# Optimization experiments

Measured on AMD Instinct MI355X. Metric: run time of the kernel, lower is better.

## Reference

```python
import jax, jax.numpy as jnp
import numpy as np

NUM_HEADS = 12


def setup_inputs() -> dict:
    key = jax.random.key(0)
    k1, k2, k3 = jax.random.split(key, 3)
    B, N, C = 2, 2048, 768
    x = jax.random.normal(k1, (B, N, C), dtype=jnp.float32)
    w_qkv = jax.random.normal(k2, (C, 3 * C), dtype=jnp.float32) * 0.02
    w_proj = jax.random.normal(k3, (C, C), dtype=jnp.float32) * 0.02
    b_proj = jnp.zeros((C,), dtype=jnp.float32)
    return {"x": x, "w_qkv": w_qkv, "w_proj": w_proj, "b_proj": b_proj}


def reference(x, w_qkv, w_proj, b_proj):
    B, N, C = x.shape
    H = NUM_HEADS
    D = C // H
    qkv = (x @ w_qkv).reshape(B, N, 3, H, D)  # [B,N,3,H,D]
    q = jnp.transpose(qkv[:, :, 0], (0, 2, 1, 3))  # [B,H,N,D]
    k = jnp.transpose(qkv[:, :, 1], (0, 2, 1, 3))
    v = jnp.transpose(qkv[:, :, 2], (0, 2, 1, 3))
    # ELU+1 feature map (note: self.scale is unused in the original forward)
    q = jax.nn.elu(q) + 1.0
    k = jax.nn.elu(k) + 1.0
    attn = jnp.einsum("bhnd,bhmd->bhnm", q, k)  # explicit O(N^2) as in source
    attn = attn / jnp.sum(attn, axis=-1, keepdims=True)
    out = jnp.einsum("bhnm,bhmd->bhnd", attn, v)  # [B,H,N,D]
    out = jnp.transpose(out, (0, 2, 1, 3)).reshape(B, N, C)
    out = out @ w_proj + b_proj
    return out, attn
```

## Files before the change

kernel.cpp:

```cpp
#include <hip/hip_runtime.h>
#include <hip/hip_bf16.h>
#include <cstdint>
#include <cmath>

#define BDIM 256

constexpr int Bb = 2;
constexpr int Nn = 2048;
constexpr int Cc = 768;
constexpr int Hh = 12;
constexpr int Dd = 64;
constexpr int TC = 3 * Cc;
constexpr int BH = Bb * Hh;
constexpr int NCHUNK = 16;
constexpr int CHROWS = Nn / NCHUNK;

typedef __attribute__((ext_vector_type(8))) short short8v;
typedef __attribute__((ext_vector_type(4))) float f32x4;

__device__ __forceinline__ float elu1(float x) {
  return x > 0.f ? x + 1.f : expf(x);
}

__device__ __forceinline__ unsigned short f2bf(float f) {
  uint32_t u = __float_as_uint(f);
  uint32_t r = (u + 0x7fff + ((u >> 16) & 1)) >> 16;
  return (unsigned short)r;
}
__device__ __forceinline__ float bf2f(unsigned short h) {
  return __uint_as_float(((uint32_t)h) << 16);
}

__device__ __forceinline__ void gll16(const unsigned short* g, unsigned short* ldsbase) {
  __builtin_amdgcn_global_load_lds((const __attribute__((address_space(1))) void*)g,
                                   (__attribute__((address_space(3))) void*)ldsbase,
                                   16, 0, 0);
}

constexpr int XBLK = 3072;
constexpr int WQBLK = (TC / 32) * (Cc / 32);
constexpr int WPBLK = (Cc / 32) * (Cc / 32);

__device__ __forceinline__ void castT_tile(const float* __restrict__ W,
                                           unsigned short* __restrict__ Wh,
                                           int K, int N, int n0, int k0, int tid,
                                           float (*t)[33]) {
  const int r = tid >> 3, c4 = (tid & 7) * 4;
  float4 v = *(const float4*)&W[(size_t)(k0 + r) * N + n0 + c4];
  t[r][c4 + 0] = v.x;
  t[r][c4 + 1] = v.y;
  t[r][c4 + 2] = v.z;
  t[r][c4 + 3] = v.w;
  __syncthreads();
  const int n = tid >> 3, k4 = (tid & 7) * 4;
  ushort4 h;
  h.x = f2bf(t[k4 + 0][n]);
  h.y = f2bf(t[k4 + 1][n]);
  h.z = f2bf(t[k4 + 2][n]);
  h.w = f2bf(t[k4 + 3][n]);
  *(ushort4*)&Wh[(size_t)(n0 + n) * K + k0 + k4] = h;
}

__global__ __launch_bounds__(BDIM) void fused_cast(const float* __restrict__ x,
                                                   const float* __restrict__ w_qkv,
                                                   const float* __restrict__ w_proj,
                                                   unsigned short* __restrict__ xh,
                                                   unsigned short* __restrict__ wqh,
                                                   unsigned short* __restrict__ wph) {
  __shared__ float t[32][33];
  const int bid = blockIdx.x, tid = threadIdx.x;
  if (bid < XBLK) {
    int i = (bid * BDIM + tid) * 4;
    float4 v = *(const float4*)&x[i];
    ushort4 h;
    h.x = f2bf(v.x);
    h.y = f2bf(v.y);
    h.z = f2bf(v.z);
    h.w = f2bf(v.w);
    *(ushort4*)&xh[i] = h;
  } else if (bid < XBLK + WQBLK) {
    int q = bid - XBLK;
    castT_tile(w_qkv, wqh, Cc, TC, (q % (TC / 32)) * 32, (q / (TC / 32)) * 32, tid, t);
  } else {
    int p = bid - XBLK - WQBLK;
    castT_tile(w_proj, wph, Cc, Cc, (p % (Cc / 32)) * 32, (p / (Cc / 32)) * 32, tid, t);
  }
}

template <int EP>
__global__ __launch_bounds__(BDIM) void mfma_k(
    const unsigned short* __restrict__ A, const unsigned short* __restrict__ Bt,
    const float* __restrict__ bias, const float* __restrict__ denom,
    float* __restrict__ C, int Mrows, int Nw, int K,
    long sAz, long sBz, long sCz,
    unsigned short* __restrict__ qpb, unsigned short* __restrict__ kpb,
    unsigned short* __restrict__ vpb) {
  __shared__ __align__(16) unsigned short lds[16384];
  __shared__ float dnls[128];

  const int z = blockIdx.z;
  const unsigned short* A0 = A + (size_t)z * sAz;
  const unsigned short* B0 = Bt + (size_t)z * sBz;
  float* Cz = C + (size_t)z * sCz;

  const int tid = threadIdx.x;
  const int wave = tid >> 6, lane = tid & 63;
  const int wr = wave >> 1, wc = wave & 1;
  const int row0 = blockIdx.y * 128, col0 = blockIdx.x * 128;
  const int l15 = lane & 15, l4 = lane >> 4;
  const int srow = wave * 16 + (lane >> 2);
  const int scol = (lane & 3) * 8;
  const int wbase = wave * 512;

  float dnv_reg = 0.f;
  if constexpr (EP == 1) dnv_reg = denom[(size_t)z * Mrows + row0 + (tid & 127)];

  auto STAGE = [&](int buf, int k0) {
    unsigned short* dst = lds + buf * 8192 + wbase;
    gll16(&A0[(size_t)(row0 + srow) * K + k0 + scol], dst);
    gll16(&A0[(size_t)(row0 + 64 + srow) * K + k0 + scol], dst + 2048);
    gll16(&B0[(size_t)(col0 + srow) * K + k0 + scol], dst + 4096);
    gll16(&B0[(size_t)(col0 + 64 + srow) * K + k0 + scol], dst + 6144);
  };

  f32x4 acc[4][4];
#pragma unroll
  for (int i = 0; i < 4; ++i)
#pragma unroll
    for (int j = 0; j < 4; ++j) acc[i][j] = {0.f, 0.f, 0.f, 0.f};

  auto COMPUTE = [&](int buf) {
    const unsigned short* la = lds + buf * 8192;
    const unsigned short* lb = la + 4096;
    short8v av[4], bv[4];
#pragma unroll
    for (int i = 0; i < 4; ++i)
      av[i] = *(const short8v*)&la[(wr * 64 + i * 16 + l15) * 32 + l4 * 8];
#pragma unroll
    for (int j = 0; j < 4; ++j)
      bv[j] = *(const short8v*)&lb[(wc * 64 + j * 16 + l15) * 32 + l4 * 8];
#pragma unroll
    for (int i = 0; i < 4; ++i)
#pragma unroll
      for (int j = 0; j < 4; ++j)
        acc[i][j] = __builtin_amdgcn_mfma_f32_16x16x32_bf16(av[i], bv[j], acc[i][j], 0, 0, 0);
  };

  const int nt = K >> 5;
  STAGE(0, 0);
  if (nt > 1) STAGE(1, 32);
  int cur = 0;
  for (int t = 0; t < nt; ++t) {
    if (t < nt - 1)
      asm volatile("s_waitcnt vmcnt(4)" ::: "memory");
    else
      asm volatile("s_waitcnt vmcnt(0)" ::: "memory");
    __builtin_amdgcn_s_barrier();
    COMPUTE(cur);
    if (t < nt - 2) {
      __builtin_amdgcn_s_barrier();
      STAGE(cur, (t + 2) * 32);
    }
    cur ^= 1;
  }

  if constexpr (EP == 0) {
#pragma unroll
    for (int i = 0; i < 4; ++i) {
      const int rbase = row0 + wr * 64 + i * 16 + l4 * 4;
#pragma unroll
      for (int j = 0; j < 4; ++j) {
        const int col = col0 + wc * 64 + j * 16 + l15;
        float bs = bias[col];
#pragma unroll
        for (int r = 0; r < 4; ++r)
          Cz[(size_t)(rbase + r) * Nw + col] = acc[i][j][r] + bs;
      }
    }
  } else if constexpr (EP == 1) {
    if (tid < 128) dnls[tid] = 1.0f / dnv_reg;
    float* fl = (float*)lds;
#pragma unroll
    for (int i = 0; i < 4; ++i) {
      __syncthreads();
#pragma unroll
      for (int j = 0; j < 4; ++j)
#pragma unroll
        for (int r = 0; r < 4; ++r)
          fl[(wr * 16 + l4 * 4 + r) * 132 + wc * 64 + j * 16 + l15] =
              acc[i][j][r] * dnls[wr * 64 + i * 16 + l4 * 4 + r];
      __syncthreads();
#pragma unroll
      for (int p = 0; p < 4; ++p) {
        int f4 = p * 256 + tid;
        int cr = f4 >> 5, c4 = (f4 & 31) * 4;
        float4 v = *(float4*)&fl[cr * 132 + c4];
        int grow = row0 + (cr >> 4) * 64 + i * 16 + (cr & 15);
        *(float4*)&Cz[(size_t)grow * Nw + col0 + c4] = v;
      }
    }
  } else {
    const int colblk = blockIdx.x;
    const int tt = colblk / 6;
    const int rcbase = (colblk % 6) * 128 + wc * 64;
#pragma unroll
    for (int i = 0; i < 4; ++i) {
      const int rowb = row0 + wr * 64 + i * 16 + l4 * 4;
#pragma unroll
      for (int j = 0; j < 4; ++j) {
        const int rc = rcbase + j * 16 + l15;
        const int h = rc >> 6, d = rc & 63;
#pragma unroll
        for (int r = 0; r < 4; ++r) {
          const int row = rowb + r;
          const int b = row >> 11, n = row & (Nn - 1);
          const size_t idx = ((size_t)(b * Hh + h) * Nn + n) * 64 + d;
          float val = acc[i][j][r];
          if (tt == 0) {
            qpb[idx] = f2bf(elu1(val));
          } else if (tt == 1) {
            kpb[idx] = f2bf(elu1(val));
          } else {
            vpb[idx] = f2bf(val);
          }
        }
      }
    }
  }
}

__global__ __launch_bounds__(BDIM) void kv_partial(const unsigned short* __restrict__ kpb,
                                                   const unsigned short* __restrict__ vpb,
                                                   float* __restrict__ kvpart,
                                                   float* __restrict__ kspart) {
  const int chunk = blockIdx.x, bh = blockIdx.y;
  __shared__ unsigned short ks[16][64];
  __shared__ unsigned short vs[16][64];
  __shared__ float ksl[16][64];
  const int tid = threadIdx.x;
  const int e = tid & 63, dg = tid >> 6;
  const int srow = tid >> 4, sd4 = (tid & 15) * 4;
  float acc[16] = {};
  float ksp[4] = {0.f, 0.f, 0.f, 0.f};
  const int n0base = chunk * CHROWS;
  for (int s = 0; s < CHROWS; s += 16) {
    const int n = n0base + s + srow;
    ushort4 kk = *(const ushort4*)&kpb[((size_t)bh * Nn + n) * 64 + sd4];
    ushort4 vv = *(const ushort4*)&vpb[((size_t)bh * Nn + n) * 64 + sd4];
    __syncthreads();
    *(ushort4*)&ks[srow][sd4] = kk;
    *(ushort4*)&vs[srow][sd4] = vv;
    ksp[0] += bf2f(kk.x);
    ksp[1] += bf2f(kk.y);
    ksp[2] += bf2f(kk.z);
    ksp[3] += bf2f(kk.w);
    __syncthreads();
#pragma unroll
    for (int j = 0; j < 16; ++j) {
      const float v = bf2f(vs[j][e]);
      short8v k8a = *(const short8v*)&ks[j][dg * 16];
      short8v k8b = *(const short8v*)&ks[j][dg * 16 + 8];
#pragma unroll
      for (int d = 0; d < 8; ++d) acc[d] += bf2f((unsigned short)k8a[d]) * v;
#pragma unroll
      for (int d = 0; d < 8; ++d) acc[8 + d] += bf2f((unsigned short)k8b[d]) * v;
    }
  }
  float* outp = kvpart + (size_t)(bh * NCHUNK + chunk) * 4096;
#pragma unroll
  for (int d = 0; d < 16; ++d) outp[(dg * 16 + d) * 64 + e] = acc[d];
  ksl[srow][sd4 + 0] = ksp[0];
  ksl[srow][sd4 + 1] = ksp[1];
  ksl[srow][sd4 + 2] = ksp[2];
  ksl[srow][sd4 + 3] = ksp[3];
  __syncthreads();
  if (tid < 64) {
    float s2 = 0.f;
#pragma unroll
    for (int r = 0; r < 16; ++r) s2 += ksl[r][tid];
    kspart[(bh * NCHUNK + chunk) * 64 + tid] = s2;
  }
}

__global__ __launch_bounds__(BDIM) void kv_reduce(const float* __restrict__ kvpart,
                                                  const float* __restrict__ kspart,
                                                  unsigned short* __restrict__ kvtb,
                                                  float* __restrict__ ksum) {
  const int seg = blockIdx.x, bh = blockIdx.y, tid = threadIdx.x;
  const int idx = seg * 256 + tid;
  float s = 0.f;
#pragma unroll 4
  for (int c = 0; c < NCHUNK; ++c) s += kvpart[(size_t)(bh * NCHUNK + c) * 4096 + idx];
  const int dk = idx >> 6, dv = idx & 63;
  kvtb[(size_t)bh * 4096 + dv * 64 + dk] = f2bf(s);
  if (tid < 4) {
    int e = seg * 4 + tid;
    float s2 = 0.f;
#pragma unroll 4
    for (int c = 0; c < NCHUNK; ++c) s2 += kspart[(bh * NCHUNK + c) * 64 + e];
    ksum[bh * 64 + e] = s2;
  }
}

__global__ __launch_bounds__(BDIM) void outpre_mfma(
    const unsigned short* __restrict__ qpb, const unsigned short* __restrict__ kvtb,
    const float* __restrict__ ksum, float* __restrict__ denom,
    unsigned short* __restrict__ oph) {
  const int nc = blockIdx.x, bh = blockIdx.y;
  const int b = bh / Hh, h = bh % Hh;
  __shared__ float kss[64];
  __shared__ float dnls[128];
  const int tid = threadIdx.x;
  const int wv = tid >> 6, lane = tid & 63;
  const int l15 = lane & 15, l4 = lane >> 4;
  if (tid < 64) kss[tid] = ksum[bh * 64 + tid];

  const int rowb = nc * 128 + wv * 32;
  const unsigned short* Aq = qpb + ((size_t)bh * Nn + rowb) * 64;
  const unsigned short* Bk = kvtb + (size_t)bh * 4096;

  short8v av[2][2], bv[4][2];
#pragma unroll
  for (int ks = 0; ks < 2; ++ks) {
#pragma unroll
    for (int i = 0; i < 2; ++i)
      av[i][ks] = *(const short8v*)&Aq[(size_t)(i * 16 + l15) * 64 + ks * 32 + l4 * 8];
#pragma unroll
    for (int j = 0; j < 4; ++j)
      bv[j][ks] = *(const short8v*)&Bk[(size_t)(j * 16 + l15) * 64 + ks * 32 + l4 * 8];
  }
  f32x4 acc[2][4];
#pragma unroll
  for (int i = 0; i < 2; ++i)
#pragma unroll
    for (int j = 0; j < 4; ++j) acc[i][j] = {0.f, 0.f, 0.f, 0.f};
#pragma unroll
  for (int ks = 0; ks < 2; ++ks)
#pragma unroll
    for (int i = 0; i < 2; ++i)
#pragma unroll
      for (int j = 0; j < 4; ++j)
        acc[i][j] = __builtin_amdgcn_mfma_f32_16x16x32_bf16(av[i][ks], bv[j][ks],
                                                            acc[i][j], 0, 0, 0);

  __syncthreads();
  float dpart[2] = {0.f, 0.f};
#pragma unroll
  for (int ks = 0; ks < 2; ++ks)
#pragma unroll
    for (int i = 0; i < 2; ++i)
#pragma unroll
      for (int t = 0; t < 8; ++t)
        dpart[i] += bf2f((unsigned short)av[i][ks][t]) * kss[ks * 32 + l4 * 8 + t];
#pragma unroll
  for (int i = 0; i < 2; ++i) {
    dpart[i] += __shfl_xor(dpart[i], 16);
    dpart[i] += __shfl_xor(dpart[i], 32);
    if (l4 == 0) {
      dnls[wv * 32 + i * 16 + l15] = dpart[i];
      denom[(size_t)bh * Nn + rowb + i * 16 + l15] = dpart[i];
    }
  }
  __syncthreads();
#pragma unroll
  for (int i = 0; i < 2; ++i) {
#pragma unroll
    for (int r = 0; r < 4; ++r) {
      const int rl = i * 16 + l4 * 4 + r;
      const float rd = 1.0f / dnls[wv * 32 + rl];
      const int nrow = rowb + rl;
#pragma unroll
      for (int j = 0; j < 4; ++j)
        oph[((size_t)b * Nn + nrow) * Cc + h * 64 + j * 16 + l15] =
            f2bf(acc[i][j][r] * rd);
    }
  }
}

extern "C" void kernel_launch(void* const* d_in, const int* in_sizes, int n_in,
                              void* d_out, int out_size, void* d_ws, size_t ws_size,
                              hipStream_t stream) {
  const float* x = (const float*)d_in[0];
  const float* w_qkv = (const float*)d_in[1];
  const float* w_proj = (const float*)d_in[2];
  const float* b_proj = (const float*)d_in[3];
  float* out = (float*)d_out;
  float* attn = out + (size_t)Bb * Nn * Cc;

  float* ws = (float*)d_ws;
  float* kvpart = ws;
  float* kspart = kvpart + 1572864;
  float* ksum = kspart + 24576;
  float* denom = ksum + 2048;
  unsigned short* us = (unsigned short*)(denom + 49152);
  unsigned short* xh = us;
  unsigned short* wqh = xh + 3145728;
  unsigned short* qpb = wqh + 1769472;
  unsigned short* kpb = qpb + 3145728;
  unsigned short* vpb = kpb + 3145728;
  unsigned short* kvtb = vpb + 3145728;
  unsigned short* oph = kvtb + 98304;
  unsigned short* wph = oph + 3145728;

  fused_cast<<<dim3(XBLK + WQBLK + WPBLK), BDIM, 0, stream>>>(x, w_qkv, w_proj, xh, wqh,
                                                              wph);
  mfma_k<2><<<dim3(TC / 128, 32, 1), BDIM, 0, stream>>>(
      xh, wqh, nullptr, nullptr, nullptr, Bb * Nn, TC, Cc, 0, 0, 0,
      qpb, kpb, vpb);
  kv_partial<<<dim3(NCHUNK, BH), BDIM, 0, stream>>>(kpb, vpb, kvpart, kspart);
  kv_reduce<<<dim3(16, BH), BDIM, 0, stream>>>(kvpart, kspart, kvtb, ksum);
  outpre_mfma<<<dim3(Nn / 128, BH), BDIM, 0, stream>>>(qpb, kvtb, ksum, denom, oph);
  mfma_k<1><<<dim3(Nn / 128, Nn / 128, BH), BDIM, 0, stream>>>(
      qpb, kpb, nullptr, denom, attn, Nn, Nn, Dd,
      (long)Nn * Dd, (long)Nn * Dd, (long)Nn * Nn,
      nullptr, nullptr, nullptr);
  mfma_k<0><<<dim3(Cc / 128, 32, 1), BDIM, 0, stream>>>(
      oph, wph, b_proj, nullptr, out, Bb * Nn, Cc, Cc, 0, 0, 0,
      nullptr, nullptr, nullptr);
}
```

Before: 172.1 us.

## Merge attention-matrix and projection GEMMs into one launch, swizzle blocks, use nontemporal stores

Turns the MFMA GEMM kernel into a device function and adds two wrapper kernels. The QKV GEMM now uses a 1D grid with an XCD-style swizzle of block ids. The attention-matrix GEMM and the output projection GEMM run in a single launch that dispatches on block index, which removes one kernel launch and lets the two run concurrently. Output stores for attn and out become nontemporal so the large 400MB-class attn write does not pollute cache; the risk is that the swizzle changes L2 locality and that mixing the block types leaves a tail imbalance.

```diff
diff --git a/kernel.cpp b/kernel.cpp
--- a/kernel.cpp
+++ b/kernel.cpp
@@ -88,32 +88,30 @@
 }
 
 template <int EP>
-__global__ __launch_bounds__(BDIM) void mfma_k(
+__device__ __forceinline__ void mfma_core(
+    int bx, int by, int bz,
     const unsigned short* __restrict__ A, const unsigned short* __restrict__ Bt,
     const float* __restrict__ bias, const float* __restrict__ denom,
     float* __restrict__ C, int Mrows, int Nw, int K,
     long sAz, long sBz, long sCz,
     unsigned short* __restrict__ qpb, unsigned short* __restrict__ kpb,
-    unsigned short* __restrict__ vpb) {
-  __shared__ __align__(16) unsigned short lds[16384];
-  __shared__ float dnls[128];
-
-  const int z = blockIdx.z;
-  const unsigned short* A0 = A + (size_t)z * sAz;
-  const unsigned short* B0 = Bt + (size_t)z * sBz;
-  float* Cz = C + (size_t)z * sCz;
+    unsigned short* __restrict__ vpb,
+    unsigned short* lds, float* dnls) {
+  const unsigned short* A0 = A + (size_t)bz * sAz;
+  const unsigned short* B0 = Bt + (size_t)bz * sBz;
+  float* Cz = C + (size_t)bz * sCz;
 
   const int tid = threadIdx.x;
   const int wave = tid >> 6, lane = tid & 63;
   const int wr = wave >> 1, wc = wave & 1;
-  const int row0 = blockIdx.y * 128, col0 = blockIdx.x * 128;
+  const int row0 = by * 128, col0 = bx * 128;
   const int l15 = lane & 15, l4 = lane >> 4;
   const int srow = wave * 16 + (lane >> 2);
   const int scol = (lane & 3) * 8;
   const int wbase = wave * 512;
 
   float dnv_reg = 0.f;
-  if constexpr (EP == 1) dnv_reg = denom[(size_t)z * Mrows + row0 + (tid & 127)];
+  if constexpr (EP == 1) dnv_reg = denom[(size_t)bz * Mrows + row0 + (tid & 127)];
 
   auto STAGE = [&](int buf, int k0) {
     unsigned short* dst = lds + buf * 8192 + wbase;
@@ -174,7 +172,8 @@
         float bs = bias[col];
 #pragma unroll
         for (int r = 0; r < 4; ++r)
-          Cz[(size_t)(rbase + r) * Nw + col] = acc[i][j][r] + bs;
+          __builtin_nontemporal_store(acc[i][j][r] + bs,
+                                      &Cz[(size_t)(rbase + r) * Nw + col]);
       }
     }
   } else if constexpr (EP == 1) {
@@ -194,15 +193,14 @@
       for (int p = 0; p < 4; ++p) {
         int f4 = p * 256 + tid;
         int cr = f4 >> 5, c4 = (f4 & 31) * 4;
-        float4 v = *(float4*)&fl[cr * 132 + c4];
+        f32x4 v = *(const f32x4*)&fl[cr * 132 + c4];
         int grow = row0 + (cr >> 4) * 64 + i * 16 + (cr & 15);
-        *(float4*)&Cz[(size_t)grow * Nw + col0 + c4] = v;
+        __builtin_nontemporal_store(v, (f32x4*)&Cz[(size_t)grow * Nw + col0 + c4]);
       }
     }
   } else {
-    const int colblk = blockIdx.x;
-    const int tt = colblk / 6;
-    const int rcbase = (colblk % 6) * 128 + wc * 64;
+    const int tt = bx / 6;
+    const int rcbase = (bx % 6) * 128 + wc * 64;
 #pragma unroll
     for (int i = 0; i < 4; ++i) {
       const int rowb = row0 + wr * 64 + i * 16 + l4 * 4;
@@ -226,6 +224,41 @@
         }
       }
     }
+  }
+}
+
+__global__ __launch_bounds__(BDIM) void gemm_qkv_k(
+    const unsigned short* __restrict__ xh, const unsigned short* __restrict__ wqh,
+    unsigned short* __restrict__ qpb, unsigned short* __restrict__ kpb,
+    unsigned short* __restrict__ vpb) {
+  __shared__ __align__(16) unsigned short lds[16384];
+  __shared__ float dnls[128];
+  const int bid = blockIdx.x;
+  const int swz = (bid & 7) * 72 + (bid >> 3);
+  const int bx = swz % 18, by = swz / 18;
+  mfma_core<2>(bx, by, 0, xh, wqh, nullptr, nullptr, nullptr, Bb * Nn, TC, Cc,
+               0, 0, 0, qpb, kpb, vpb, lds, dnls);
+}
+
+__global__ __launch_bounds__(BDIM) void attn_proj_k(
+    const unsigned short* __restrict__ qpb, const unsigned short* __restrict__ kpb,
+    const float* __restrict__ denom, float* __restrict__ attn,
+    const unsigned short* __restrict__ oph, const unsigned short* __restrict__ wph,
+    const float* __restrict__ b_proj, float* __restrict__ out) {
+  __shared__ __align__(16) unsigned short lds[16384];
+  __shared__ float dnls[128];
+  const int bid = blockIdx.x;
+  if (bid < 6144) {
+    const int swz = (bid & 7) * 768 + (bid >> 3);
+    const int bz = swz >> 8, rem = swz & 255;
+    const int by = rem >> 4, bx = rem & 15;
+    mfma_core<1>(bx, by, bz, qpb, kpb, nullptr, denom, attn, Nn, Nn, Dd,
+                 (long)Nn * Dd, (long)Nn * Dd, (long)Nn * Nn,
+                 nullptr, nullptr, nullptr, lds, dnls);
+  } else {
+    const int p = bid - 6144;
+    mfma_core<0>(p % 6, p / 6, 0, oph, wph, b_proj, nullptr, out, Bb * Nn, Cc, Cc,
+                 0, 0, 0, nullptr, nullptr, nullptr, lds, dnls);
   }
 }
 
@@ -404,17 +437,10 @@
 
   fused_cast<<<dim3(XBLK + WQBLK + WPBLK), BDIM, 0, stream>>>(x, w_qkv, w_proj, xh, wqh,
                                                               wph);
-  mfma_k<2><<<dim3(TC / 128, 32, 1), BDIM, 0, stream>>>(
-      xh, wqh, nullptr, nullptr, nullptr, Bb * Nn, TC, Cc, 0, 0, 0,
-      qpb, kpb, vpb);
+  gemm_qkv_k<<<dim3(576), BDIM, 0, stream>>>(xh, wqh, qpb, kpb, vpb);
   kv_partial<<<dim3(NCHUNK, BH), BDIM, 0, stream>>>(kpb, vpb, kvpart, kspart);
   kv_reduce<<<dim3(16, BH), BDIM, 0, stream>>>(kvpart, kspart, kvtb, ksum);
   outpre_mfma<<<dim3(Nn / 128, BH), BDIM, 0, stream>>>(qpb, kvtb, ksum, denom, oph);
-  mfma_k<1><<<dim3(Nn / 128, Nn / 128, BH), BDIM, 0, stream>>>(
-      qpb, kpb, nullptr, denom, attn, Nn, Nn, Dd,
-      (long)Nn * Dd, (long)Nn * Dd, (long)Nn * Nn,
-      nullptr, nullptr, nullptr);
-  mfma_k<0><<<dim3(Cc / 128, 32, 1), BDIM, 0, stream>>>(
-      oph, wph, b_proj, nullptr, out, Bb * Nn, Cc, Cc, 0, 0, 0,
-      nullptr, nullptr, nullptr);
-}
+  attn_proj_k<<<dim3(6144 + 192), BDIM, 0, stream>>>(qpb, kpb, denom, attn,
+                                                     oph, wph, b_proj, out);
+}
```

New measurement: 149.7 us (median of 2 runs). 13.0% less time.
